# Kernel tuning notes

Measured on AMD Instinct MI355X. Metric: run time of the kernel, lower is better.

## Reference

```python
import jax, jax.numpy as jnp
import numpy as np

B, S, D, H = 2, 2048, 1024, 16
HD = D // H


def setup_inputs() -> dict:
    key = jax.random.key(0)
    ks = jax.random.split(key, 9)
    s = 1.0 / np.sqrt(D)
    return {
        "x": jax.random.normal(ks[0], (B, S, D), dtype=jnp.float32),
        "Wq": jax.random.uniform(ks[1], (D, D), jnp.float32, -s, s),
        "bq": jax.random.uniform(ks[2], (D,), jnp.float32, -s, s),
        "Wk": jax.random.uniform(ks[3], (D, D), jnp.float32, -s, s),
        "bk": jax.random.uniform(ks[4], (D,), jnp.float32, -s, s),
        "Wv": jax.random.uniform(ks[5], (D, D), jnp.float32, -s, s),
        "bv": jax.random.uniform(ks[6], (D,), jnp.float32, -s, s),
        "Wo": jax.random.uniform(ks[7], (D, D), jnp.float32, -s, s),
        "bo": jax.random.uniform(ks[8], (D,), jnp.float32, -s, s),
    }


def reference(x, Wq, bq, Wk, bk, Wv, bv, Wo, bo):
    # QKV projections: [B,S,D] -> [B,H,S,HD]
    def split_heads(t):
        return t.reshape(B, S, H, HD).transpose(0, 2, 1, 3)

    Q = split_heads(x @ Wq + bq)
    K = split_heads(x @ Wk + bk)
    V = split_heads(x @ Wv + bv)

    scale = 1.0 / np.sqrt(HD).astype(np.float32)
    scores = jnp.einsum("bhqd,bhkd->bhqk", Q, K) * scale  # [B,H,S,S]
    attn = jax.nn.softmax(scores, axis=-1)
    out = jnp.einsum("bhqk,bhkd->bhqd", attn, V)  # [B,H,S,HD]
    out = out.transpose(0, 2, 1, 3).reshape(B, S, D)
    return out @ Wo + bo
```

## Files before the change

kernel.cpp:

```cpp
#include <hip/hip_runtime.h>
#include <hip/hip_bf16.h>

#define B_ 2
#define S_ 2048
#define D_ 1024
#define H_ 16
#define HD_ 64
#define M_ (B_ * S_)

#define SC2L 0.18033688011112042f

typedef __attribute__((ext_vector_type(8))) short short8;
typedef __attribute__((ext_vector_type(4))) float f32x4;
using bf16_t = __hip_bfloat16;

__device__ __forceinline__ float fast_exp2(float x) { return __builtin_amdgcn_exp2f(x); }

__device__ __forceinline__ short f2bfs(float f) {
    __hip_bfloat16 h = __float2bfloat16(f);
    return *reinterpret_cast<short*>(&h);
}

typedef __attribute__((address_space(1))) const unsigned int gl_u32;
typedef __attribute__((address_space(3))) unsigned int lds_u32;

__device__ __forceinline__ void gl_lds16(const bf16_t* g, bf16_t* l) {
    __builtin_amdgcn_global_load_lds((gl_u32*)g, (lds_u32*)l, 16, 0, 0);
}

__device__ __forceinline__ int swzb(int row, int colbyte) {
    return (row << 7) + (colbyte ^ ((row & 7) << 4));
}

__device__ __forceinline__ int swz32(int row, int chunk) {
    return (row << 6) + ((chunk ^ ((row >> 1) & 3)) << 4);
}

__global__ __launch_bounds__(256) void k_transpose_w4(const float* __restrict__ W0,
                                                      const float* __restrict__ W1,
                                                      const float* __restrict__ W2,
                                                      const float* __restrict__ W3,
                                                      bf16_t* T0, bf16_t* T1, bf16_t* T2, bf16_t* T3) {
    __shared__ float tile[32][33];
    const int z = blockIdx.z;
    const float* W = z == 0 ? W0 : z == 1 ? W1 : z == 2 ? W2 : W3;
    bf16_t* Wt = z == 0 ? T0 : z == 1 ? T1 : z == 2 ? T2 : T3;
    const int tx = threadIdx.x, ty = threadIdx.y;
    const int n0 = blockIdx.x * 32, k0 = blockIdx.y * 32;
#pragma unroll
    for (int r = 0; r < 4; ++r)
        tile[ty + 8 * r][tx] = W[(size_t)(k0 + ty + 8 * r) * D_ + n0 + tx];
    __syncthreads();
#pragma unroll
    for (int r = 0; r < 4; ++r)
        Wt[(size_t)(n0 + ty + 8 * r) * D_ + k0 + tx] = __float2bfloat16(tile[tx][ty + 8 * r]);
}

__global__ __launch_bounds__(256) void k_x2bf(const float* __restrict__ x, bf16_t* __restrict__ xb) {
    const int i = blockIdx.x * 2048 + threadIdx.x * 8;
    float4 f0 = ((const float4*)(x + i))[0];
    float4 f1 = ((const float4*)(x + i))[1];
    short8 v;
    v[0] = f2bfs(f0.x); v[1] = f2bfs(f0.y); v[2] = f2bfs(f0.z); v[3] = f2bfs(f0.w);
    v[4] = f2bfs(f1.x); v[5] = f2bfs(f1.y); v[6] = f2bfs(f1.z); v[7] = f2bfs(f1.w);
    *(short8*)(xb + i) = v;
}

__device__ __forceinline__ void stage_pair32(const bf16_t* __restrict__ Asrc,
                                             const bf16_t* __restrict__ Bsrc,
                                             int k0, int tid,
                                             bf16_t* Ab, bf16_t* Bb) {
#pragma unroll
    for (int c = 0; c < 2; ++c) {
        int idx = c * 256 + tid;
        int r = idx >> 2, ch = idx & 3;
        int cs = ch ^ ((r >> 1) & 3);
        gl_lds16(Asrc + (size_t)r * D_ + k0 + cs * 8, Ab + idx * 8);
        gl_lds16(Bsrc + (size_t)r * D_ + k0 + cs * 8, Bb + idx * 8);
    }
}

__device__ __forceinline__ void gemm_compute32(const bf16_t* Ab, const bf16_t* Bb,
                                               int lane, int wr, int wc, f32x4 acc[4][4]) {
    const char* AbC = (const char*)Ab;
    const char* BbC = (const char*)Bb;
    const int g = lane >> 4;
    short8 af[4], bf[4];
    const int arow = wr * 64 + (lane & 15);
    const int brow = wc * 64 + (lane & 15);
#pragma unroll
    for (int i = 0; i < 4; ++i) af[i] = *(const short8*)(AbC + swz32(arow + i * 16, g));
#pragma unroll
    for (int j = 0; j < 4; ++j) bf[j] = *(const short8*)(BbC + swz32(brow + j * 16, g));
#pragma unroll
    for (int i = 0; i < 4; ++i)
#pragma unroll
        for (int j = 0; j < 4; ++j)
            acc[i][j] = __builtin_amdgcn_mfma_f32_16x16x32_bf16(af[i], bf[j], acc[i][j], 0, 0, 0);
}

__global__ __launch_bounds__(256, 4) void k_qkv(const bf16_t* __restrict__ xb,
                                                const bf16_t* __restrict__ Wtq,
                                                const bf16_t* __restrict__ Wtk,
                                                const bf16_t* __restrict__ Wtv,
                                                const float* __restrict__ bq,
                                                const float* __restrict__ bk,
                                                const float* __restrict__ bv,
                                                bf16_t* __restrict__ Qh,
                                                bf16_t* __restrict__ Kh,
                                                bf16_t* __restrict__ Vt) {
    __shared__ __align__(16) bf16_t Ab[2][128 * 32];
    __shared__ __align__(16) bf16_t Bb[2][128 * 32];
    const int sel = blockIdx.x >> 3;
    const bf16_t* Bt = sel == 0 ? Wtq : sel == 1 ? Wtk : Wtv;
    const float* bias = sel == 0 ? bq : sel == 1 ? bk : bv;
    const int col0 = (blockIdx.x & 7) * 128;
    const int row0 = blockIdx.y * 128;
    const int tid = threadIdx.x, lane = tid & 63, w = tid >> 6;
    const int wr = w >> 1, wc = w & 1;
    const bf16_t* Asrc = xb + (size_t)row0 * D_;
    const bf16_t* Bsrc = Bt + (size_t)col0 * D_;

    f32x4 acc[4][4];
#pragma unroll
    for (int i = 0; i < 4; ++i)
#pragma unroll
        for (int j = 0; j < 4; ++j) acc[i][j] = (f32x4){0.f, 0.f, 0.f, 0.f};

    stage_pair32(Asrc, Bsrc, 0, tid, Ab[0], Bb[0]);
    constexpr int NS = D_ / 32;
#pragma unroll 2
    for (int step = 0; step < NS; ++step) {
        const int cur = step & 1;
        __syncthreads();
        if (step + 1 < NS)
            stage_pair32(Asrc, Bsrc, (step + 1) * 32, tid, Ab[cur ^ 1], Bb[cur ^ 1]);
        gemm_compute32(Ab[cur], Bb[cur], lane, wr, wc, acc);
    }

#pragma unroll
    for (int i = 0; i < 4; ++i)
#pragma unroll
        for (int j = 0; j < 4; ++j)
#pragma unroll
            for (int r = 0; r < 4; ++r) {
                int grow = row0 + wr * 64 + i * 16 + 4 * (lane >> 4) + r;
                int gcol = col0 + wc * 64 + j * 16 + (lane & 15);
                float v = acc[i][j][r] + bias[gcol];
                int b = grow >> 11, s = grow & (S_ - 1);
                int h = gcol >> 6, hd = gcol & (HD_ - 1);
                if (sel == 0)
                    Qh[(((size_t)b * H_ + h) * S_ + s) * HD_ + hd] = __float2bfloat16(v * SC2L);
                else if (sel == 1)
                    Kh[(((size_t)b * H_ + h) * S_ + s) * HD_ + hd] = __float2bfloat16(v);
                else
                    Vt[(((size_t)b * H_ + h) * HD_ + hd) * S_ + s] = __float2bfloat16(v);
            }
}

__global__ __launch_bounds__(256, 4) void k_gemm_out(const bf16_t* __restrict__ AO,
                                                     const bf16_t* __restrict__ Wto,
                                                     const float* __restrict__ bo,
                                                     float* __restrict__ out) {
    __shared__ __align__(16) bf16_t Ab[2][128 * 32];
    __shared__ __align__(16) bf16_t Bb[2][128 * 32];
    const int col0 = blockIdx.x * 128;
    const int row0 = blockIdx.y * 128;
    const int tid = threadIdx.x, lane = tid & 63, w = tid >> 6;
    const int wr = w >> 1, wc = w & 1;
    const bf16_t* Asrc = AO + (size_t)row0 * D_;
    const bf16_t* Bsrc = Wto + (size_t)col0 * D_;

    f32x4 acc[4][4];
#pragma unroll
    for (int i = 0; i < 4; ++i)
#pragma unroll
        for (int j = 0; j < 4; ++j) acc[i][j] = (f32x4){0.f, 0.f, 0.f, 0.f};

    stage_pair32(Asrc, Bsrc, 0, tid, Ab[0], Bb[0]);
    constexpr int NS = D_ / 32;
#pragma unroll 2
    for (int step = 0; step < NS; ++step) {
        const int cur = step & 1;
        __syncthreads();
        if (step + 1 < NS)
            stage_pair32(Asrc, Bsrc, (step + 1) * 32, tid, Ab[cur ^ 1], Bb[cur ^ 1]);
        gemm_compute32(Ab[cur], Bb[cur], lane, wr, wc, acc);
    }

#pragma unroll
    for (int i = 0; i < 4; ++i)
#pragma unroll
        for (int j = 0; j < 4; ++j)
#pragma unroll
            for (int r = 0; r < 4; ++r) {
                int grow = row0 + wr * 64 + i * 16 + 4 * (lane >> 4) + r;
                int gcol = col0 + wc * 64 + j * 16 + (lane & 15);
                out[(size_t)grow * D_ + gcol] = acc[i][j][r] + bo[gcol];
            }
}

__global__ __launch_bounds__(512, 4) void k_attn(const bf16_t* __restrict__ Qh,
                                                 const bf16_t* __restrict__ Kh,
                                                 const bf16_t* __restrict__ Vt,
                                                 bf16_t* __restrict__ AO) {
    constexpr int NT = S_ / 64;
    __shared__ __align__(16) bf16_t Kb[3][64 * 64];
    __shared__ __align__(16) bf16_t Vb[3][64 * 64];
    __shared__ __align__(16) bf16_t Pt[8][16 * 64];
    const int tid = threadIdx.x, lane = tid & 63, w = tid >> 6;
    const int g = lane >> 4, q = lane & 15;
    const int bid = blockIdx.x;
    const int swz = (bid & 7) * 64 + (bid >> 3);
    const int qt = swz & 15, bh = swz >> 4;
    const int h = bh & 15, b = bh >> 4;
    const bf16_t* Qbase = Qh + ((size_t)bh * S_ + qt * 128 + w * 16) * HD_;
    const bf16_t* Kbase = Kh + (size_t)bh * S_ * HD_;
    const bf16_t* Vbase = Vt + (size_t)bh * HD_ * S_;
    char* PtC = (char*)Pt[w];

    auto stage = [&](int buf, int kt) {
        int r = tid >> 3, s = tid & 7;
        int lsw = s ^ (r & 7);
        gl_lds16(Kbase + (size_t)(kt * 64 + r) * HD_ + lsw * 8, &Kb[buf][tid * 8]);
        gl_lds16(Vbase + (size_t)r * S_ + kt * 64 + lsw * 8, &Vb[buf][tid * 8]);
    };

    short8 qf[2];
#pragma unroll
    for (int kc = 0; kc < 2; ++kc)
        qf[kc] = *(const short8*)(Qbase + (size_t)q * HD_ + kc * 32 + 8 * g);

    f32x4 ls4 = (f32x4){0.f, 0.f, 0.f, 0.f};
    f32x4 o[4];
#pragma unroll
    for (int c = 0; c < 4; ++c) o[c] = (f32x4){0.f, 0.f, 0.f, 0.f};

    f32x4 scA[4], scB[4];

    auto qk_tile = [&](int kt, f32x4 (&sc)[4]) {
        const char* KbC = (const char*)Kb[kt % 3];
        __builtin_amdgcn_s_setprio(1);
#pragma unroll
        for (int ktb = 0; ktb < 4; ++ktb) {
            f32x4 a = (f32x4){0.f, 0.f, 0.f, 0.f};
#pragma unroll
            for (int kc = 0; kc < 2; ++kc) {
                short8 kf = *(const short8*)(KbC + swzb(ktb * 16 + q, kc * 64 + 16 * g));
                a = __builtin_amdgcn_mfma_f32_16x16x32_bf16(kf, qf[kc], a, 0, 0, 0);
            }
            sc[ktb] = a;
        }
        __builtin_amdgcn_s_setprio(0);
    };

    auto finish_pv = [&](f32x4 (&sc)[4], int vt) {
#pragma unroll
        for (int t = 0; t < 4; ++t)
#pragma unroll
            for (int r = 0; r < 4; ++r)
                sc[t][r] = fast_exp2(sc[t][r]);
        ls4 += (sc[0] + sc[1]) + (sc[2] + sc[3]);
#pragma unroll
        for (int t = 0; t < 4; ++t) {
            short4 pk;
            pk.x = f2bfs(sc[t][0]); pk.y = f2bfs(sc[t][1]);
            pk.z = f2bfs(sc[t][2]); pk.w = f2bfs(sc[t][3]);
            *(short4*)(PtC + swzb(q, t * 32 + 8 * g)) = pk;
        }
        const char* VbC = (const char*)Vb[vt % 3];
        __builtin_amdgcn_s_setprio(1);
#pragma unroll
        for (int kc = 0; kc < 2; ++kc) {
            short8 pf = *(const short8*)(PtC + swzb(q, kc * 64 + 16 * g));
#pragma unroll
            for (int c = 0; c < 4; ++c) {
                short8 vf = *(const short8*)(VbC + swzb(c * 16 + q, kc * 64 + 16 * g));
                o[c] = __builtin_amdgcn_mfma_f32_16x16x32_bf16(vf, pf, o[c], 0, 0, 0);
            }
        }
        __builtin_amdgcn_s_setprio(0);
    };

    stage(0, 0);
    __syncthreads();
    stage(1, 1);
    qk_tile(0, scA);

#pragma unroll 1
    for (int kt = 1; kt + 1 < NT; kt += 2) {
        __syncthreads();
        stage((kt + 1) % 3, kt + 1);
        qk_tile(kt, scB);
        finish_pv(scA, kt - 1);
        __syncthreads();
        if (kt + 2 < NT) stage((kt + 2) % 3, kt + 2);
        qk_tile(kt + 1, scA);
        finish_pv(scB, kt);
    }
    __syncthreads();
    qk_tile(NT - 1, scB);
    finish_pv(scA, NT - 2);
    finish_pv(scB, NT - 1);

    float lsum = (ls4[0] + ls4[1]) + (ls4[2] + ls4[3]);
    lsum += __shfl_xor(lsum, 16);
    lsum += __shfl_xor(lsum, 32);
    float rls = __builtin_amdgcn_rcpf(lsum);
#pragma unroll
    for (int c = 0; c < 4; ++c) {
        short4 ok;
        ok.x = f2bfs(o[c][0] * rls); ok.y = f2bfs(o[c][1] * rls);
        ok.z = f2bfs(o[c][2] * rls); ok.w = f2bfs(o[c][3] * rls);
        *(short4*)(PtC + swzb(q, c * 32 + 8 * g)) = ok;
    }
    const int tok = qt * 128 + w * 16 + (lane >> 2);
    const int dch = (lane & 3) * 32;
    short8 r0 = *(const short8*)(PtC + swzb(lane >> 2, dch));
    short8 r1 = *(const short8*)(PtC + swzb(lane >> 2, dch + 16));
    bf16_t* dst = AO + ((size_t)b * S_ + tok) * D_ + h * HD_ + (lane & 3) * 16;
    *(short8*)dst = r0;
    *(short8*)(dst + 8) = r1;
}

extern "C" void kernel_launch(void* const* d_in, const int* in_sizes, int n_in,
                              void* d_out, int out_size, void* d_ws, size_t ws_size,
                              hipStream_t stream) {
    const float* x  = (const float*)d_in[0];
    const float* Wq = (const float*)d_in[1];
    const float* bq = (const float*)d_in[2];
    const float* Wk = (const float*)d_in[3];
    const float* bk = (const float*)d_in[4];
    const float* Wv = (const float*)d_in[5];
    const float* bv = (const float*)d_in[6];
    const float* Wo = (const float*)d_in[7];
    const float* bo = (const float*)d_in[8];

    char* ws = (char*)d_ws;
    const size_t MB = 1024 * 1024;
    bf16_t* Wtq = (bf16_t*)(ws + 0 * MB);
    bf16_t* Wtk = (bf16_t*)(ws + 2 * MB);
    bf16_t* Wtv = (bf16_t*)(ws + 4 * MB);
    bf16_t* Wto = (bf16_t*)(ws + 6 * MB);
    bf16_t* xb  = (bf16_t*)(ws + 8 * MB);
    bf16_t* Qh  = (bf16_t*)(ws + 16 * MB);
    bf16_t* Kh  = (bf16_t*)(ws + 24 * MB);
    bf16_t* Vt  = (bf16_t*)(ws + 32 * MB);
    bf16_t* AO  = (bf16_t*)(ws + 8 * MB);

    k_transpose_w4<<<dim3(32, 32, 4), dim3(32, 8), 0, stream>>>(Wq, Wk, Wv, Wo, Wtq, Wtk, Wtv, Wto);
    k_x2bf<<<2048, 256, 0, stream>>>(x, xb);
    k_qkv<<<dim3(24, 32), 256, 0, stream>>>(xb, Wtq, Wtk, Wtv, bq, bk, bv, Qh, Kh, Vt);
    k_attn<<<B_ * H_ * (S_ / 128), 512, 0, stream>>>(Qh, Kh, Vt, AO);
    k_gemm_out<<<dim3(8, 32), 256, 0, stream>>>(AO, Wto, bo, (float*)d_out);
}
```

Measured before the change: 120.8 us.

## Give each attention wave two query tiles to reuse K/V fragments

The attention kernel now runs 4 waves of 256 threads per block, each handling 32 query rows (two 16-row halves) instead of 16. Each K and V fragment read from LDS then feeds two MFMAs, halving LDS reads per unit of compute. The triple-buffered, software-pipelined QK/PV schedule is replaced by a simple double-buffered loop with one barrier per tile. The risks are higher register pressure, fewer waves per block, and less overlap between the exp/softmax step and the MFMA work.

Measured after the change: 124.2 us. +2.9%, slower.

```diff
diff --git a/kernel.cpp b/kernel.cpp
--- a/kernel.cpp
+++ b/kernel.cpp
@@ -200,127 +200,139 @@
             }
 }
 
-__global__ __launch_bounds__(512, 4) void k_attn(const bf16_t* __restrict__ Qh,
+__global__ __launch_bounds__(256, 3) void k_attn(const bf16_t* __restrict__ Qh,
                                                  const bf16_t* __restrict__ Kh,
                                                  const bf16_t* __restrict__ Vt,
                                                  bf16_t* __restrict__ AO) {
     constexpr int NT = S_ / 64;
-    __shared__ __align__(16) bf16_t Kb[3][64 * 64];
-    __shared__ __align__(16) bf16_t Vb[3][64 * 64];
-    __shared__ __align__(16) bf16_t Pt[8][16 * 64];
+    __shared__ __align__(16) bf16_t Kb[2][64 * 64];
+    __shared__ __align__(16) bf16_t Vb[2][64 * 64];
+    __shared__ __align__(16) bf16_t Pt[4][32 * 64];
     const int tid = threadIdx.x, lane = tid & 63, w = tid >> 6;
     const int g = lane >> 4, q = lane & 15;
     const int bid = blockIdx.x;
     const int swz = (bid & 7) * 64 + (bid >> 3);
     const int qt = swz & 15, bh = swz >> 4;
     const int h = bh & 15, b = bh >> 4;
-    const bf16_t* Qbase = Qh + ((size_t)bh * S_ + qt * 128 + w * 16) * HD_;
+    const bf16_t* Qbase = Qh + ((size_t)bh * S_ + qt * 128 + w * 32) * HD_;
     const bf16_t* Kbase = Kh + (size_t)bh * S_ * HD_;
     const bf16_t* Vbase = Vt + (size_t)bh * HD_ * S_;
     char* PtC = (char*)Pt[w];
 
     auto stage = [&](int buf, int kt) {
-        int r = tid >> 3, s = tid & 7;
-        int lsw = s ^ (r & 7);
-        gl_lds16(Kbase + (size_t)(kt * 64 + r) * HD_ + lsw * 8, &Kb[buf][tid * 8]);
-        gl_lds16(Vbase + (size_t)r * S_ + kt * 64 + lsw * 8, &Vb[buf][tid * 8]);
+#pragma unroll
+        for (int c = 0; c < 2; ++c) {
+            int idx = c * 256 + tid;
+            int r = idx >> 3, s = idx & 7;
+            int lsw = s ^ (r & 7);
+            gl_lds16(Kbase + (size_t)(kt * 64 + r) * HD_ + lsw * 8, &Kb[buf][idx * 8]);
+            gl_lds16(Vbase + (size_t)r * S_ + kt * 64 + lsw * 8, &Vb[buf][idx * 8]);
+        }
     };
 
-    short8 qf[2];
-#pragma unroll
-    for (int kc = 0; kc < 2; ++kc)
-        qf[kc] = *(const short8*)(Qbase + (size_t)q * HD_ + kc * 32 + 8 * g);
-
-    f32x4 ls4 = (f32x4){0.f, 0.f, 0.f, 0.f};
-    f32x4 o[4];
-#pragma unroll
-    for (int c = 0; c < 4; ++c) o[c] = (f32x4){0.f, 0.f, 0.f, 0.f};
-
-    f32x4 scA[4], scB[4];
-
-    auto qk_tile = [&](int kt, f32x4 (&sc)[4]) {
-        const char* KbC = (const char*)Kb[kt % 3];
+    short8 qf[2][2];
+#pragma unroll
+    for (int qh = 0; qh < 2; ++qh)
+#pragma unroll
+        for (int kc = 0; kc < 2; ++kc)
+            qf[qh][kc] = *(const short8*)(Qbase + (size_t)(qh * 16 + q) * HD_ + kc * 32 + 8 * g);
+
+    f32x4 ls4[2];
+    f32x4 o[2][4];
+#pragma unroll
+    for (int qh = 0; qh < 2; ++qh) {
+        ls4[qh] = (f32x4){0.f, 0.f, 0.f, 0.f};
+#pragma unroll
+        for (int c = 0; c < 4; ++c) o[qh][c] = (f32x4){0.f, 0.f, 0.f, 0.f};
+    }
+
+    f32x4 sc[2][4];
+
+    stage(0, 0);
+    __syncthreads();
+
+#pragma unroll 1
+    for (int kt = 0; kt < NT; ++kt) {
+        const int cur = kt & 1;
+        if (kt + 1 < NT) stage(cur ^ 1, kt + 1);
+        const char* KbC = (const char*)Kb[cur];
+        const char* VbC = (const char*)Vb[cur];
+
         __builtin_amdgcn_s_setprio(1);
 #pragma unroll
         for (int ktb = 0; ktb < 4; ++ktb) {
-            f32x4 a = (f32x4){0.f, 0.f, 0.f, 0.f};
+            f32x4 a0 = (f32x4){0.f, 0.f, 0.f, 0.f};
+            f32x4 a1 = (f32x4){0.f, 0.f, 0.f, 0.f};
 #pragma unroll
             for (int kc = 0; kc < 2; ++kc) {
                 short8 kf = *(const short8*)(KbC + swzb(ktb * 16 + q, kc * 64 + 16 * g));
-                a = __builtin_amdgcn_mfma_f32_16x16x32_bf16(kf, qf[kc], a, 0, 0, 0);
-            }
-            sc[ktb] = a;
+                a0 = __builtin_amdgcn_mfma_f32_16x16x32_bf16(kf, qf[0][kc], a0, 0, 0, 0);
+                a1 = __builtin_amdgcn_mfma_f32_16x16x32_bf16(kf, qf[1][kc], a1, 0, 0, 0);
+            }
+            sc[0][ktb] = a0;
+            sc[1][ktb] = a1;
         }
         __builtin_amdgcn_s_setprio(0);
-    };
-
-    auto finish_pv = [&](f32x4 (&sc)[4], int vt) {
-#pragma unroll
-        for (int t = 0; t < 4; ++t)
-#pragma unroll
-            for (int r = 0; r < 4; ++r)
-                sc[t][r] = fast_exp2(sc[t][r]);
-        ls4 += (sc[0] + sc[1]) + (sc[2] + sc[3]);
-#pragma unroll
-        for (int t = 0; t < 4; ++t) {
-            short4 pk;
-            pk.x = f2bfs(sc[t][0]); pk.y = f2bfs(sc[t][1]);
-            pk.z = f2bfs(sc[t][2]); pk.w = f2bfs(sc[t][3]);
-            *(short4*)(PtC + swzb(q, t * 32 + 8 * g)) = pk;
-        }
-        const char* VbC = (const char*)Vb[vt % 3];
+
+#pragma unroll
+        for (int qh = 0; qh < 2; ++qh) {
+#pragma unroll
+            for (int t = 0; t < 4; ++t)
+#pragma unroll
+                for (int r = 0; r < 4; ++r)
+                    sc[qh][t][r] = fast_exp2(sc[qh][t][r]);
+            ls4[qh] += (sc[qh][0] + sc[qh][1]) + (sc[qh][2] + sc[qh][3]);
+        }
+
+#pragma unroll
+        for (int qh = 0; qh < 2; ++qh)
+#pragma unroll
+            for (int t = 0; t < 4; ++t) {
+                short4 pk;
+                pk.x = f2bfs(sc[qh][t][0]); pk.y = f2bfs(sc[qh][t][1]);
+                pk.z = f2bfs(sc[qh][t][2]); pk.w = f2bfs(sc[qh][t][3]);
+                *(short4*)(PtC + swzb(qh * 16 + q, t * 32 + 8 * g)) = pk;
+            }
+
         __builtin_amdgcn_s_setprio(1);
 #pragma unroll
         for (int kc = 0; kc < 2; ++kc) {
-            short8 pf = *(const short8*)(PtC + swzb(q, kc * 64 + 16 * g));
+            short8 pf0 = *(const short8*)(PtC + swzb(q, kc * 64 + 16 * g));
+            short8 pf1 = *(const short8*)(PtC + swzb(16 + q, kc * 64 + 16 * g));
 #pragma unroll
             for (int c = 0; c < 4; ++c) {
                 short8 vf = *(const short8*)(VbC + swzb(c * 16 + q, kc * 64 + 16 * g));
-                o[c] = __builtin_amdgcn_mfma_f32_16x16x32_bf16(vf, pf, o[c], 0, 0, 0);
+                o[0][c] = __builtin_amdgcn_mfma_f32_16x16x32_bf16(vf, pf0, o[0][c], 0, 0, 0);
+                o[1][c] = __builtin_amdgcn_mfma_f32_16x16x32_bf16(vf, pf1, o[1][c], 0, 0, 0);
             }
         }
         __builtin_amdgcn_s_setprio(0);
-    };
-
-    stage(0, 0);
-    __syncthreads();
-    stage(1, 1);
-    qk_tile(0, scA);
-
-#pragma unroll 1
-    for (int kt = 1; kt + 1 < NT; kt += 2) {
         __syncthreads();
-        stage((kt + 1) % 3, kt + 1);
-        qk_tile(kt, scB);
-        finish_pv(scA, kt - 1);
-        __syncthreads();
-        if (kt + 2 < NT) stage((kt + 2) % 3, kt + 2);
-        qk_tile(kt + 1, scA);
-        finish_pv(scB, kt);
-    }
-    __syncthreads();
-    qk_tile(NT - 1, scB);
-    finish_pv(scA, NT - 2);
-    finish_pv(scB, NT - 1);
-
-    float lsum = (ls4[0] + ls4[1]) + (ls4[2] + ls4[3]);
-    lsum += __shfl_xor(lsum, 16);
-    lsum += __shfl_xor(lsum, 32);
-    float rls = __builtin_amdgcn_rcpf(lsum);
-#pragma unroll
-    for (int c = 0; c < 4; ++c) {
-        short4 ok;
-        ok.x = f2bfs(o[c][0] * rls); ok.y = f2bfs(o[c][1] * rls);
-        ok.z = f2bfs(o[c][2] * rls); ok.w = f2bfs(o[c][3] * rls);
-        *(short4*)(PtC + swzb(q, c * 32 + 8 * g)) = ok;
-    }
-    const int tok = qt * 128 + w * 16 + (lane >> 2);
-    const int dch = (lane & 3) * 32;
-    short8 r0 = *(const short8*)(PtC + swzb(lane >> 2, dch));
-    short8 r1 = *(const short8*)(PtC + swzb(lane >> 2, dch + 16));
-    bf16_t* dst = AO + ((size_t)b * S_ + tok) * D_ + h * HD_ + (lane & 3) * 16;
-    *(short8*)dst = r0;
-    *(short8*)(dst + 8) = r1;
+    }
+
+#pragma unroll
+    for (int qh = 0; qh < 2; ++qh) {
+        float lsum = (ls4[qh][0] + ls4[qh][1]) + (ls4[qh][2] + ls4[qh][3]);
+        lsum += __shfl_xor(lsum, 16);
+        lsum += __shfl_xor(lsum, 32);
+        float rls = __builtin_amdgcn_rcpf(lsum);
+#pragma unroll
+        for (int c = 0; c < 4; ++c) {
+            short4 ok;
+            ok.x = f2bfs(o[qh][c][0] * rls); ok.y = f2bfs(o[qh][c][1] * rls);
+            ok.z = f2bfs(o[qh][c][2] * rls); ok.w = f2bfs(o[qh][c][3] * rls);
+            *(short4*)(PtC + swzb(qh * 16 + q, c * 32 + 8 * g)) = ok;
+        }
+    }
+    const int row = lane >> 1;
+    const int halfb = (lane & 1) * 64;
+    const int tok = qt * 128 + w * 32 + row;
+    bf16_t* dst = AO + ((size_t)b * S_ + tok) * D_ + h * HD_ + (lane & 1) * 32;
+#pragma unroll
+    for (int c2 = 0; c2 < 4; ++c2) {
+        short8 rr = *(const short8*)(PtC + swzb(row, halfb + c2 * 16));
+        *(short8*)(dst + c2 * 8) = rr;
+    }
 }
 
 extern "C" void kernel_launch(void* const* d_in, const int* in_sizes, int n_in,
@@ -351,6 +363,6 @@
     k_transpose_w4<<<dim3(32, 32, 4), dim3(32, 8), 0, stream>>>(Wq, Wk, Wv, Wo, Wtq, Wtk, Wtv, Wto);
     k_x2bf<<<2048, 256, 0, stream>>>(x, xb);
     k_qkv<<<dim3(24, 32), 256, 0, stream>>>(xb, Wtq, Wtk, Wtv, bq, bk, bv, Qh, Kh, Vt);
-    k_attn<<<B_ * H_ * (S_ / 128), 512, 0, stream>>>(Qh, Kh, Vt, AO);
+    k_attn<<<B_ * H_ * (S_ / 128), 256, 0, stream>>>(Qh, Kh, Vt, AO);
     k_gemm_out<<<dim3(8, 32), 256, 0, stream>>>(AO, Wto, bo, (float*)d_out);
 }
```
